# Optimization experiments

Hardware: AMD Instinct MI355X
Metric: run time of the kernel (lower is better)

Reference implementation:

```python
import jax, jax.numpy as jnp
import numpy as np
import math

D_MODEL = 1024
NUM_HEADS = 16
HEAD_DIM = D_MODEL // NUM_HEADS
ROPE_THETA = 10000.0
MAX_SEQ_LEN = 4096


def setup_inputs() -> dict:
    key = jax.random.key(0)
    ks = jax.random.split(key, 6)
    sigma = math.sqrt(2.0 / (D_MODEL + D_MODEL))
    def w(k):
        # trunc_normal within [-3sigma, 3sigma] ~ approximate with clipped normal
        return jnp.clip(sigma * jax.random.normal(k, (D_MODEL, D_MODEL), dtype=jnp.float32), -3 * sigma, 3 * sigma)
    x = jax.random.normal(ks[0], (2, 2048, D_MODEL), dtype=jnp.float32)
    token_positions = jnp.arange(2048, dtype=jnp.int64 if jax.config.jax_enable_x64 else jnp.int32)
    return {
        "x": x,
        "wq": w(ks[1]),
        "wk": w(ks[2]),
        "wv": w(ks[3]),
        "wo": w(ks[4]),
        "token_positions": token_positions,
    }


def _rope(t, positions):
    # t: (B, H, S, head_dim); positions: (S,)
    half = HEAD_DIM // 2
    inv_freq = 1.0 / (ROPE_THETA ** (jnp.arange(0, HEAD_DIM, 2, dtype=jnp.float32) / HEAD_DIM))  # (half,)
    freqs = positions.astype(jnp.float32)[:, None] * inv_freq[None, :]  # (S, half)
    cos = jnp.cos(freqs)
    sin = jnp.sin(freqs)
    t_even = t[..., ::2]   # (B,H,S,half)
    t_odd = t[..., 1::2]
    rot_even = t_even * cos - t_odd * sin
    rot_odd = t_even * sin + t_odd * cos
    return jnp.stack([rot_even, rot_odd], axis=-1).reshape(t.shape)


def reference(x, wq, wk, wv, wo, token_positions):
    B, S, _ = x.shape
    def split_heads(t):
        return t.reshape(B, S, NUM_HEADS, HEAD_DIM).transpose(0, 2, 1, 3)  # (B,H,S,Dh)
    q = split_heads(jnp.einsum('bsd,ed->bse', x, wq))
    k = split_heads(jnp.einsum('bsd,ed->bse', x, wk))
    v = split_heads(jnp.einsum('bsd,ed->bse', x, wv))
    q = _rope(q, token_positions)
    k = _rope(k, token_positions)
    scores = jnp.einsum('bhqd,bhkd->bhqk', q, k) / math.sqrt(HEAD_DIM)
    causal = jnp.tril(jnp.ones((S, S), dtype=bool))
    scores = jnp.where(causal, scores, -jnp.inf)
    probs = jax.nn.softmax(scores, axis=-1)
    out = jnp.einsum('bhqk,bhkd->bhqd', probs, v)  # (B,H,S,Dh)
    out = out.transpose(0, 2, 1, 3).reshape(B, S, D_MODEL)
    return jnp.einsum('bsd,ed->bse', out, wo)
```

## Files before the change

### kernel.cpp

```cpp
#include <hip/hip_runtime.h>
#include <hip/hip_bf16.h>


#define D_MODEL 1024
#define NHEADS  16
#define HDIM    64
#define SEQ     2048
#define BATCH   2

typedef unsigned short u16;
typedef __bf16 bf16x8_t __attribute__((ext_vector_type(8)));
typedef float  f32x4_t  __attribute__((ext_vector_type(4)));

__device__ __forceinline__ u16 f2bf(float f) {
    union { __hip_bfloat16 h; u16 u; } cv;
    cv.h = __float2bfloat16(f);
    return cv.u;
}

__device__ __forceinline__ unsigned pk2(float x, float y) {
    union { __hip_bfloat162 h; unsigned u; } cv;
    cv.h = __float22bfloat162_rn(make_float2(x, y));
    return cv.u;
}

__device__ __forceinline__ uint4 pack8(float4 a, float4 b) {
    uint4 u;
    u.x = pk2(a.x, a.y);
    u.y = pk2(a.z, a.w);
    u.z = pk2(b.x, b.y);
    u.w = pk2(b.z, b.w);
    return u;
}

__device__ __forceinline__ bf16x8_t frag_ld(const u16* p) {
    union { uint4 u; bf16x8_t v; } t;
    t.u = *(const uint4*)p;
    return t.v;
}

__device__ __forceinline__ void acc8(uint4 u, float* a) {
    a[0] += __uint_as_float(u.x << 16); a[1] += __uint_as_float(u.x & 0xffff0000u);
    a[2] += __uint_as_float(u.y << 16); a[3] += __uint_as_float(u.y & 0xffff0000u);
    a[4] += __uint_as_float(u.z << 16); a[5] += __uint_as_float(u.z & 0xffff0000u);
    a[6] += __uint_as_float(u.w << 16); a[7] += __uint_as_float(u.w & 0xffff0000u);
}

__device__ __forceinline__ void dma16(const u16* g, u16* l) {
    __builtin_amdgcn_global_load_lds(
        (const __attribute__((address_space(1))) void*)g,
        (__attribute__((address_space(3))) void*)l, 16, 0, 0);
}

__global__ __launch_bounds__(256) void conv_bf16_kernel(
    const float* __restrict__ X, const float* __restrict__ Wq,
    const float* __restrict__ Wk, const float* __restrict__ Wv,
    const float* __restrict__ Wo, u16* __restrict__ Xbf, u16* __restrict__ Wbf)
{
    const size_t gid = (size_t)blockIdx.x * 256 + threadIdx.x;
    const float* src;
    u16* dst;
    size_t off;
    if (gid < (1u << 19)) {
        src = X; dst = Xbf; off = gid;
    } else {
        size_t g = gid - (1u << 19);
        const int wsel = (int)(g >> 17);
        g &= (1u << 17) - 1;
        src = (wsel == 0) ? Wq : (wsel == 1) ? Wk : (wsel == 2) ? Wv : Wo;
        dst = Wbf + ((size_t)wsel << 20);
        off = g;
    }
    const float4 a = *(const float4*)(src + off * 8);
    const float4 b = *(const float4*)(src + off * 8 + 4);
    *(uint4*)(dst + off * 8) = pack8(a, b);
}

__global__ __launch_bounds__(256) void qkv_rope_kernel(
    const u16* __restrict__ Xbf, const u16* __restrict__ Wbf,
    const int* __restrict__ pos,
    u16* __restrict__ Qo, u16* __restrict__ Ko, u16* __restrict__ Vt)
{
    __shared__ __align__(16) u16 smem[16896];
    u16* As = smem;
    u16* Bs = smem + 8192;

    const int tid = threadIdx.x;
    const int m0 = blockIdx.y * 128;
    const int nv = blockIdx.x * 128;
    const int which = nv >> 10;
    const int nbase = nv & 1023;
    const u16* __restrict__ Wsrc = Wbf + ((size_t)which << 20);

    const int w = tid >> 6, L = tid & 63, quad = L >> 4, colL = L & 15;
    const int mw = (w & 1) * 64, nw = (w >> 1) * 64;

    const int lrow = L >> 3;
    const int lchk = (L & 7) ^ lrow;
    const u16* ag = Xbf + (size_t)(m0 + 32 * w + lrow) * D_MODEL + lchk * 8;
    const u16* bg = Wsrc + (size_t)(nbase + 32 * w + lrow) * D_MODEL + lchk * 8;
    u16* al = As + (32 * w) * 64;
    u16* bl = Bs + (32 * w) * 64;

    f32x4_t acc[4][4];
    #pragma unroll
    for (int i = 0; i < 4; ++i)
        #pragma unroll
        for (int j = 0; j < 4; ++j) acc[i][j] = (f32x4_t){0.f, 0.f, 0.f, 0.f};

    for (int k0 = 0; k0 < D_MODEL; k0 += 64) {
        __syncthreads();
        #pragma unroll
        for (int j = 0; j < 4; ++j) {
            dma16(ag + (size_t)j * 8 * D_MODEL + k0, al + j * 512);
            dma16(bg + (size_t)j * 8 * D_MODEL + k0, bl + j * 512);
        }
        __syncthreads();
        #pragma unroll
        for (int kb = 0; kb < 2; ++kb) {
            const int ch = ((kb * 4 + quad) ^ (colL & 7)) * 8;
            bf16x8_t af[4], bf[4];
            #pragma unroll
            for (int t = 0; t < 4; ++t) {
                af[t] = frag_ld(As + (mw + t * 16 + colL) * 64 + ch);
                bf[t] = frag_ld(Bs + (nw + t * 16 + colL) * 64 + ch);
            }
            #pragma unroll
            for (int mt = 0; mt < 4; ++mt)
                #pragma unroll
                for (int nt = 0; nt < 4; ++nt)
                    acc[mt][nt] = __builtin_amdgcn_mfma_f32_16x16x32_bf16(
                        af[mt], bf[nt], acc[mt][nt], 0, 0, 0);
        }
    }

    __syncthreads();
    u16 (*Ts)[132] = (u16(*)[132])smem;

    const float C0 = 0.14391156831212787f;
    if (which < 2) {
        const float oscale = (which == 0) ? 0.18033688011112042f : 1.0f;
        float invf[4], sgn[4];
        #pragma unroll
        for (int nt = 0; nt < 4; ++nt) {
            const int n = nbase + nw + nt * 16 + colL;
            const int dd = n & 63;
            invf[nt] = __expf(-(float)(dd & 62) * C0);
            sgn[nt] = (dd & 1) ? 1.0f : -1.0f;
        }
        #pragma unroll
        for (int mt = 0; mt < 4; ++mt) {
            #pragma unroll
            for (int r = 0; r < 4; ++r) {
                const int ml = mw + mt * 16 + quad * 4 + r;
                const int ss = (m0 + ml) & 2047;
                const float p = (float)pos[ss];
                #pragma unroll
                for (int nt = 0; nt < 4; ++nt) {
                    const float v = acc[mt][nt][r];
                    const float partner = __shfl_xor(v, 1);
                    float sn, cs;
                    __sincosf(p * invf[nt], &sn, &cs);
                    Ts[ml][nw + nt * 16 + colL] =
                        f2bf((v * cs + sgn[nt] * sn * partner) * oscale);
                }
            }
        }
    } else {
        #pragma unroll
        for (int mt = 0; mt < 4; ++mt)
            #pragma unroll
            for (int nt = 0; nt < 4; ++nt)
                #pragma unroll
                for (int r = 0; r < 4; ++r)
                    Ts[nw + nt * 16 + colL][mw + mt * 16 + quad * 4 + r] = f2bf(acc[mt][nt][r]);
    }
    __syncthreads();

    const int rr0 = tid >> 4;
    const int cc8 = (tid & 15) * 8;
    if (which < 2) {
        u16* __restrict__ dst = (which == 0) ? Qo : Ko;
        #pragma unroll
        for (int it = 0; it < 8; ++it) {
            const int ml = rr0 + it * 16;
            const int m = m0 + ml, bb = m >> 11, ss = m & 2047;
            const int n = nbase + cc8, h = n >> 6, d = n & 63;
            *(uint4*)&dst[((size_t)(bb * NHEADS + h) * SEQ + ss) * HDIM + d] =
                *(const uint4*)&Ts[ml][cc8];
        }
    } else {
        const int bb = m0 >> 11, ss0 = (m0 & 2047) + cc8;
        #pragma unroll
        for (int it = 0; it < 8; ++it) {
            const int nl = rr0 + it * 16;
            const int n = nbase + nl, h = n >> 6, d = n & 63;
            *(uint4*)&Vt[((size_t)(bb * NHEADS + h) * HDIM + d) * SEQ + ss0] =
                *(const uint4*)&Ts[nl][cc8];
        }
    }
}

__global__ __launch_bounds__(256) void attn_kernel(
    const u16* __restrict__ Q, const u16* __restrict__ K,
    const u16* __restrict__ Vt, u16* __restrict__ Opart, float* __restrict__ Lpart)
{
    __shared__ __align__(16) u16 Ks[64][72];
    __shared__ __align__(16) u16 Vs[64][72];
    __shared__ __align__(16) u16 Ps[4][16][72];

    const int tid = threadIdx.x;
    const int slot = 79 - (int)blockIdx.x;
    const int g = (slot >= 48) ? 3 : (slot >= 24) ? 2 : (slot >= 8) ? 1 : 0;
    const int t0 = slot - 4 * g * (g + 1);
    const int rr = t0 / (g + 1);
    const int s  = t0 - rr * (g + 1);
    const int qt = 8 * g + rr;

    const int hh = blockIdx.y, bb = blockIdx.z;
    const size_t bh = ((size_t)bb * NHEADS + hh) * (SEQ * HDIM);
    const int q0 = qt * 64;
    const int kt0 = s * 8;
    const int ktend = min(kt0 + 8, qt + 1);
    const size_t gslot = ((size_t)(bb * NHEADS + hh) * 80 + slot);

    const int w = tid >> 6, L = tid & 63, quad = L >> 4, colL = L & 15;
    const int srow = tid >> 2, sc = (tid & 3) * 16;

    const u16* qp = Q + bh + (size_t)(q0 + w * 16 + colL) * HDIM + quad * 8;
    const bf16x8_t aq0 = frag_ld(qp);
    const bf16x8_t aq1 = frag_ld(qp + 32);

    float lsum = 0.f;
    f32x4_t O[4];
    #pragma unroll
    for (int dt = 0; dt < 4; ++dt) O[dt] = (f32x4_t){0.f, 0.f, 0.f, 0.f};

    const u16* kp = K + bh + (size_t)(kt0 * 64 + srow) * HDIM + sc;
    const u16* vp = Vt + bh + (size_t)srow * SEQ + kt0 * 64 + sc;
    uint4 kv0 = *(const uint4*)kp;
    uint4 kv1 = *(const uint4*)(kp + 8);
    uint4 vv0 = *(const uint4*)vp;
    uint4 vv1 = *(const uint4*)(vp + 8);

    for (int kt = kt0; kt < ktend; ++kt) {
        __builtin_amdgcn_s_barrier();
        asm volatile("s_waitcnt vmcnt(0)" ::: "memory");
        __builtin_amdgcn_sched_barrier(0);
        *(uint4*)&Ks[srow][sc]     = kv0;
        *(uint4*)&Ks[srow][sc + 8] = kv1;
        *(uint4*)&Vs[srow][sc]     = vv0;
        *(uint4*)&Vs[srow][sc + 8] = vv1;
        if (kt + 1 < ktend) {
            const int k1 = (kt + 1) * 64;
            const u16* kpn = K + bh + (size_t)(k1 + srow) * HDIM + sc;
            kv0 = *(const uint4*)kpn;
            kv1 = *(const uint4*)(kpn + 8);
            const u16* vpn = Vt + bh + (size_t)srow * SEQ + k1 + sc;
            vv0 = *(const uint4*)vpn;
            vv1 = *(const uint4*)(vpn + 8);
        }
        asm volatile("s_waitcnt lgkmcnt(0)" ::: "memory");
        __builtin_amdgcn_sched_barrier(0);
        __builtin_amdgcn_s_barrier();

        const bool diag = (kt == qt);
        const int ntmax = diag ? w : 3;
        const int kbmax = diag ? (w >> 1) : 1;

        f32x4_t S[4];
        #pragma unroll
        for (int nt = 0; nt < 4; ++nt) S[nt] = (f32x4_t){0.f, 0.f, 0.f, 0.f};
        #pragma unroll
        for (int nt = 0; nt < 4; ++nt) {
            if (nt <= ntmax) {
                S[nt] = __builtin_amdgcn_mfma_f32_16x16x32_bf16(
                    frag_ld(&Ks[nt * 16 + colL][quad * 8]), aq0, S[nt], 0, 0, 0);
                S[nt] = __builtin_amdgcn_mfma_f32_16x16x32_bf16(
                    frag_ld(&Ks[nt * 16 + colL][32 + quad * 8]), aq1, S[nt], 0, 0, 0);
            }
        }

        if (!diag) {
            #pragma unroll
            for (int nt = 0; nt < 4; ++nt) {
                const float p0 = __builtin_amdgcn_exp2f(S[nt][0]);
                const float p1 = __builtin_amdgcn_exp2f(S[nt][1]);
                const float p2 = __builtin_amdgcn_exp2f(S[nt][2]);
                const float p3 = __builtin_amdgcn_exp2f(S[nt][3]);
                lsum += (p0 + p1) + (p2 + p3);
                uint2 pw;
                pw.x = pk2(p0, p1);
                pw.y = pk2(p2, p3);
                *(uint2*)&Ps[w][colL][nt * 16 + quad * 4] = pw;
            }
        } else {
            const int qrel = w * 16 + colL;
            #pragma unroll
            for (int nt = 0; nt < 4; ++nt) {
                float p0 = 0.f, p1 = 0.f, p2 = 0.f, p3 = 0.f;
                if (nt <= ntmax) {
                    const int krel = nt * 16 + quad * 4;
                    p0 = (krel + 0 <= qrel) ? __builtin_amdgcn_exp2f(S[nt][0]) : 0.f;
                    p1 = (krel + 1 <= qrel) ? __builtin_amdgcn_exp2f(S[nt][1]) : 0.f;
                    p2 = (krel + 2 <= qrel) ? __builtin_amdgcn_exp2f(S[nt][2]) : 0.f;
                    p3 = (krel + 3 <= qrel) ? __builtin_amdgcn_exp2f(S[nt][3]) : 0.f;
                }
                lsum += (p0 + p1) + (p2 + p3);
                uint2 pw;
                pw.x = pk2(p0, p1);
                pw.y = pk2(p2, p3);
                *(uint2*)&Ps[w][colL][nt * 16 + quad * 4] = pw;
            }
        }

        asm volatile("s_waitcnt lgkmcnt(0)" ::: "memory");
        __builtin_amdgcn_sched_barrier(0);

        #pragma unroll
        for (int kb = 0; kb < 2; ++kb) {
            if (kb <= kbmax) {
                const bf16x8_t ap = frag_ld(&Ps[w][colL][kb * 32 + quad * 8]);
                #pragma unroll
                for (int dt = 0; dt < 4; ++dt) {
                    const bf16x8_t bv = frag_ld(&Vs[dt * 16 + colL][kb * 32 + quad * 8]);
                    O[dt] = __builtin_amdgcn_mfma_f32_16x16x32_bf16(ap, bv, O[dt], 0, 0, 0);
                }
            }
        }
    }

    {
        float sm = lsum;
        sm += __shfl_xor(sm, 16);
        sm += __shfl_xor(sm, 32);
        if (quad == 0)
            Lpart[gslot * 64 + 16 * w + colL] = sm;
    }

    #pragma unroll
    for (int dt = 0; dt < 4; ++dt)
        #pragma unroll
        for (int r = 0; r < 4; ++r)
            Ps[w][quad * 4 + r][dt * 16 + colL] = f2bf(O[dt][r]);
    asm volatile("s_waitcnt lgkmcnt(0)" ::: "memory");
    __builtin_amdgcn_sched_barrier(0);
    #pragma unroll
    for (int p = 0; p < 2; ++p) {
        const int rowl = (L >> 3) + 8 * p;
        const int c8 = (L & 7) * 8;
        *(uint4*)&Opart[gslot * 4096 + (size_t)(16 * w + rowl) * 64 + c8] =
            *(const uint4*)&Ps[w][rowl][c8];
    }
}

__global__ __launch_bounds__(256) void combine_kernel(
    const u16* __restrict__ Opart, const float* __restrict__ Lpart,
    u16* __restrict__ AO)
{
    const int qt = blockIdx.x, hh = blockIdx.y, bb = blockIdx.z;
    const int g = qt >> 3;
    const int nsplit = g + 1;
    const int base = 4 * g * (g + 1) + (qt & 7) * (g + 1);
    const int t = threadIdx.x;
    const int q = t >> 2, dg = (t & 3) * 16;
    const size_t slot0 = (size_t)(bb * NHEADS + hh) * 80 + base;

    float acc[16];
    #pragma unroll
    for (int i = 0; i < 16; ++i) acc[i] = 0.f;
    float l = 0.f;
    for (int s = 0; s < nsplit; ++s) {
        const size_t gs = slot0 + s;
        l += Lpart[gs * 64 + q];
        const u16* op = Opart + gs * 4096 + (size_t)q * 64 + dg;
        acc8(*(const uint4*)op, acc);
        acc8(*(const uint4*)(op + 8), acc + 8);
    }
    const float inv = 1.0f / l;
    uint4 o0, o1;
    o0.x = pk2(acc[0] * inv, acc[1] * inv);  o0.y = pk2(acc[2] * inv, acc[3] * inv);
    o0.z = pk2(acc[4] * inv, acc[5] * inv);  o0.w = pk2(acc[6] * inv, acc[7] * inv);
    o1.x = pk2(acc[8] * inv, acc[9] * inv);  o1.y = pk2(acc[10] * inv, acc[11] * inv);
    o1.z = pk2(acc[12] * inv, acc[13] * inv); o1.w = pk2(acc[14] * inv, acc[15] * inv);
    u16* dst = AO + ((size_t)bb * SEQ + qt * 64 + q) * D_MODEL + hh * HDIM + dg;
    *(uint4*)dst = o0;
    *(uint4*)(dst + 8) = o1;
}

__global__ __launch_bounds__(256) void out_proj_kernel(
    const u16* __restrict__ A, const u16* __restrict__ Wob, float* __restrict__ Out)
{
    __shared__ __align__(16) u16 smem[16384];
    u16* As = smem;
    u16* Bs = smem + 8192;

    const int tid = threadIdx.x;
    const int m0 = blockIdx.y * 128;
    const int n0 = blockIdx.x * 128;

    const int w = tid >> 6, L = tid & 63, quad = L >> 4, colL = L & 15;
    const int mw = (w & 1) * 64, nw = (w >> 1) * 64;

    const int lrow = L >> 3;
    const int lchk = (L & 7) ^ lrow;
    const u16* ag = A + (size_t)(m0 + 32 * w + lrow) * D_MODEL + lchk * 8;
    const u16* bg = Wob + (size_t)(n0 + 32 * w + lrow) * D_MODEL + lchk * 8;
    u16* al = As + (32 * w) * 64;
    u16* bl = Bs + (32 * w) * 64;

    f32x4_t acc[4][4];
    #pragma unroll
    for (int i = 0; i < 4; ++i)
        #pragma unroll
        for (int j = 0; j < 4; ++j) acc[i][j] = (f32x4_t){0.f, 0.f, 0.f, 0.f};

    for (int k0 = 0; k0 < D_MODEL; k0 += 64) {
        __syncthreads();
        #pragma unroll
        for (int j = 0; j < 4; ++j) {
            dma16(ag + (size_t)j * 8 * D_MODEL + k0, al + j * 512);
            dma16(bg + (size_t)j * 8 * D_MODEL + k0, bl + j * 512);
        }
        __syncthreads();
        #pragma unroll
        for (int kb = 0; kb < 2; ++kb) {
            const int ch = ((kb * 4 + quad) ^ (colL & 7)) * 8;
            bf16x8_t af[4], bf[4];
            #pragma unroll
            for (int t = 0; t < 4; ++t) {
                af[t] = frag_ld(As + (mw + t * 16 + colL) * 64 + ch);
                bf[t] = frag_ld(Bs + (nw + t * 16 + colL) * 64 + ch);
            }
            #pragma unroll
            for (int mt = 0; mt < 4; ++mt)
                #pragma unroll
                for (int nt = 0; nt < 4; ++nt)
                    acc[mt][nt] = __builtin_amdgcn_mfma_f32_16x16x32_bf16(
                        af[mt], bf[nt], acc[mt][nt], 0, 0, 0);
        }
    }

    #pragma unroll
    for (int mt = 0; mt < 4; ++mt)
        #pragma unroll
        for (int nt = 0; nt < 4; ++nt)
            #pragma unroll
            for (int r = 0; r < 4; ++r) {
                const int m = m0 + mw + mt * 16 + quad * 4 + r;
                const int n = n0 + nw + nt * 16 + colL;
                Out[(size_t)m * D_MODEL + n] = acc[mt][nt][r];
            }
}

extern "C" void kernel_launch(void* const* d_in, const int* in_sizes, int n_in,
                              void* d_out, int out_size, void* d_ws, size_t ws_size,
                              hipStream_t stream) {
    const float* x  = (const float*)d_in[0];
    const float* wq = (const float*)d_in[1];
    const float* wk = (const float*)d_in[2];
    const float* wv = (const float*)d_in[3];
    const float* wo = (const float*)d_in[4];
    const int* pos  = (const int*)d_in[5];
    float* out = (float*)d_out;

    const size_t NELEM = (size_t)BATCH * NHEADS * SEQ * HDIM;
    u16* Qw  = (u16*)d_ws;
    u16* Kw  = Qw + NELEM;
    u16* Vtw = Kw + NELEM;
    u16* AOw = Vtw + NELEM;
    u16* Xbf = AOw;
    u16* Wbf = AOw + NELEM;
    u16* Opart = Wbf + NELEM;
    float* Lpart = (float*)(Opart + (size_t)2560 * 4096);

    conv_bf16_kernel<<<4096, 256, 0, stream>>>(x, wq, wk, wv, wo, Xbf, Wbf);
    qkv_rope_kernel<<<dim3(24, 32), 256, 0, stream>>>(Xbf, Wbf, pos, Qw, Kw, Vtw);
    attn_kernel<<<dim3(80, NHEADS, BATCH), 256, 0, stream>>>(Qw, Kw, Vtw, Opart, Lpart);
    combine_kernel<<<dim3(32, NHEADS, BATCH), 256, 0, stream>>>(Opart, Lpart, AOw);
    out_proj_kernel<<<dim3(8, 32), 256, 0, stream>>>(AOw, Wbf + 3 * (1u << 20), out);
}
```

Before: 192.9 us.

## Double-buffer LDS tiles in QKV and output projection GEMMs

Both projection GEMM kernels now keep two LDS stages and issue the async global-to-LDS copies for the next k-tile before computing on the current one. Partial vmcnt waits and raw s_barrier replace the two __syncthreads per iteration. The aim is to hide global load latency behind MFMA work. In exchange, LDS use per block doubles to 64KB, which may reduce occupancy.

```diff
diff --git a/kernel.cpp b/kernel.cpp
--- a/kernel.cpp
+++ b/kernel.cpp
@@ -81,10 +81,7 @@
     const int* __restrict__ pos,
     u16* __restrict__ Qo, u16* __restrict__ Ko, u16* __restrict__ Vt)
 {
-    __shared__ __align__(16) u16 smem[16896];
-    u16* As = smem;
-    u16* Bs = smem + 8192;
-
+    __shared__ __align__(16) u16 smem[32768];
     const int tid = threadIdx.x;
     const int m0 = blockIdx.y * 128;
     const int nv = blockIdx.x * 128;
@@ -99,8 +96,6 @@
     const int lchk = (L & 7) ^ lrow;
     const u16* ag = Xbf + (size_t)(m0 + 32 * w + lrow) * D_MODEL + lchk * 8;
     const u16* bg = Wsrc + (size_t)(nbase + 32 * w + lrow) * D_MODEL + lchk * 8;
-    u16* al = As + (32 * w) * 64;
-    u16* bl = Bs + (32 * w) * 64;
 
     f32x4_t acc[4][4];
     #pragma unroll
@@ -108,22 +103,40 @@
         #pragma unroll
         for (int j = 0; j < 4; ++j) acc[i][j] = (f32x4_t){0.f, 0.f, 0.f, 0.f};
 
-    for (int k0 = 0; k0 < D_MODEL; k0 += 64) {
-        __syncthreads();
-        #pragma unroll
-        for (int j = 0; j < 4; ++j) {
-            dma16(ag + (size_t)j * 8 * D_MODEL + k0, al + j * 512);
-            dma16(bg + (size_t)j * 8 * D_MODEL + k0, bl + j * 512);
-        }
-        __syncthreads();
+    #define QKV_STAGE(boff, k0)                                                 \
+        {                                                                       \
+            u16* al = smem + (boff) + (32 * w) * 64;                            \
+            u16* bl = smem + 16384 + (boff) + (32 * w) * 64;                    \
+            _Pragma("unroll")                                                   \
+            for (int j = 0; j < 4; ++j) {                                       \
+                dma16(ag + (size_t)j * 8 * D_MODEL + (k0), al + j * 512);       \
+                dma16(bg + (size_t)j * 8 * D_MODEL + (k0), bl + j * 512);       \
+            }                                                                   \
+        }
+
+    QKV_STAGE(0, 0)
+    for (int it = 0; it < 16; ++it) {
+        const int boff = (it & 1) << 13;
+        if (it < 15) {
+            QKV_STAGE(boff ^ 8192, (it + 1) * 64)
+            asm volatile("s_waitcnt vmcnt(8)" ::: "memory");
+        } else {
+            asm volatile("s_waitcnt vmcnt(0)" ::: "memory");
+        }
+        __builtin_amdgcn_sched_barrier(0);
+        __builtin_amdgcn_s_barrier();
+        __builtin_amdgcn_sched_barrier(0);
+
+        const u16* a_s = smem + boff;
+        const u16* b_s = smem + 16384 + boff;
         #pragma unroll
         for (int kb = 0; kb < 2; ++kb) {
             const int ch = ((kb * 4 + quad) ^ (colL & 7)) * 8;
             bf16x8_t af[4], bf[4];
             #pragma unroll
             for (int t = 0; t < 4; ++t) {
-                af[t] = frag_ld(As + (mw + t * 16 + colL) * 64 + ch);
-                bf[t] = frag_ld(Bs + (nw + t * 16 + colL) * 64 + ch);
+                af[t] = frag_ld(a_s + (mw + t * 16 + colL) * 64 + ch);
+                bf[t] = frag_ld(b_s + (nw + t * 16 + colL) * 64 + ch);
             }
             #pragma unroll
             for (int mt = 0; mt < 4; ++mt)
@@ -132,6 +145,7 @@
                     acc[mt][nt] = __builtin_amdgcn_mfma_f32_16x16x32_bf16(
                         af[mt], bf[nt], acc[mt][nt], 0, 0, 0);
         }
+        __builtin_amdgcn_s_barrier();
     }
 
     __syncthreads();
@@ -391,9 +405,7 @@
 __global__ __launch_bounds__(256) void out_proj_kernel(
     const u16* __restrict__ A, const u16* __restrict__ Wob, float* __restrict__ Out)
 {
-    __shared__ __align__(16) u16 smem[16384];
-    u16* As = smem;
-    u16* Bs = smem + 8192;
+    __shared__ __align__(16) u16 smem[32768];
 
     const int tid = threadIdx.x;
     const int m0 = blockIdx.y * 128;
@@ -406,8 +418,6 @@
     const int lchk = (L & 7) ^ lrow;
     const u16* ag = A + (size_t)(m0 + 32 * w + lrow) * D_MODEL + lchk * 8;
     const u16* bg = Wob + (size_t)(n0 + 32 * w + lrow) * D_MODEL + lchk * 8;
-    u16* al = As + (32 * w) * 64;
-    u16* bl = Bs + (32 * w) * 64;
 
     f32x4_t acc[4][4];
     #pragma unroll
@@ -415,22 +425,29 @@
         #pragma unroll
         for (int j = 0; j < 4; ++j) acc[i][j] = (f32x4_t){0.f, 0.f, 0.f, 0.f};
 
-    for (int k0 = 0; k0 < D_MODEL; k0 += 64) {
-        __syncthreads();
-        #pragma unroll
-        for (int j = 0; j < 4; ++j) {
-            dma16(ag + (size_t)j * 8 * D_MODEL + k0, al + j * 512);
-            dma16(bg + (size_t)j * 8 * D_MODEL + k0, bl + j * 512);
-        }
-        __syncthreads();
+    QKV_STAGE(0, 0)
+    for (int it = 0; it < 16; ++it) {
+        const int boff = (it & 1) << 13;
+        if (it < 15) {
+            QKV_STAGE(boff ^ 8192, (it + 1) * 64)
+            asm volatile("s_waitcnt vmcnt(8)" ::: "memory");
+        } else {
+            asm volatile("s_waitcnt vmcnt(0)" ::: "memory");
+        }
+        __builtin_amdgcn_sched_barrier(0);
+        __builtin_amdgcn_s_barrier();
+        __builtin_amdgcn_sched_barrier(0);
+
+        const u16* a_s = smem + boff;
+        const u16* b_s = smem + 16384 + boff;
         #pragma unroll
         for (int kb = 0; kb < 2; ++kb) {
             const int ch = ((kb * 4 + quad) ^ (colL & 7)) * 8;
             bf16x8_t af[4], bf[4];
             #pragma unroll
             for (int t = 0; t < 4; ++t) {
-                af[t] = frag_ld(As + (mw + t * 16 + colL) * 64 + ch);
-                bf[t] = frag_ld(Bs + (nw + t * 16 + colL) * 64 + ch);
+                af[t] = frag_ld(a_s + (mw + t * 16 + colL) * 64 + ch);
+                bf[t] = frag_ld(b_s + (nw + t * 16 + colL) * 64 + ch);
             }
             #pragma unroll
             for (int mt = 0; mt < 4; ++mt)
@@ -439,6 +456,7 @@
                     acc[mt][nt] = __builtin_amdgcn_mfma_f32_16x16x32_bf16(
                         af[mt], bf[nt], acc[mt][nt], 0, 0, 0);
         }
+        __builtin_amdgcn_s_barrier();
     }
 
     #pragma unroll
```

After: 194.0 us. No clear change (+0.5%).
